# Kernel tuning notes

Measured on AMD Instinct MI355X. Metric: run time of the kernel, lower is better.

Reference implementation:

```python
import jax, jax.numpy as jnp
import numpy as np

SCORE_THRESHOLD = 0.15
IOU_THRESHOLD = 0.5
MAX_OUTPUT = 10          # tf.image.non_max_suppression(..., 10, ...)
NUM_CLASSES = 80
NUM_ANCHORS = 5
NEG = -1e9               # score for suppressed / below-threshold boxes


def setup_inputs() -> dict:
    key = jax.random.key(0)
    k1, k2 = jax.random.split(key)
    preds = jax.random.normal(k1, (16, 52, 52, NUM_ANCHORS * (5 + NUM_CLASSES)), dtype=jnp.float32)
    # anchor priors in grid-cell units, typical YOLOv2 range
    anchors = jax.random.uniform(k2, (NUM_ANCHORS, 2), dtype=jnp.float32, minval=0.5, maxval=6.0)
    return {"preds": preds, "anchors": anchors}


def _decode(preds, anchors):
    """YOLOv2 head decode (the `_interpret_prediction` callable)."""
    B, H, W, _ = preds.shape
    A = anchors.shape[0]
    p = preds.reshape(B, H, W, A, 5 + NUM_CLASSES)
    gy, gx = jnp.meshgrid(jnp.arange(H, dtype=preds.dtype),
                          jnp.arange(W, dtype=preds.dtype), indexing="ij")
    grid = jnp.stack([gx, gy], axis=-1)[None, :, :, None, :]   # (1,H,W,1,2) in (x,y)
    dims = jnp.array([W, H], dtype=preds.dtype)
    box_xy = (jax.nn.sigmoid(p[..., :2]) + grid) / dims        # normalized centers
    box_wh = jnp.exp(p[..., 2:4]) * anchors[None, None, None, :, :] / dims
    box_confidence = jax.nn.sigmoid(p[..., 4:5])
    box_class_probs = jax.nn.softmax(p[..., 5:], axis=-1)
    return box_xy, box_wh, box_confidence, box_class_probs


def _iou(box, boxes):
    """IoU of one box (ymin,xmin,ymax,xmax) against all boxes [N,4]."""
    tl = jnp.maximum(box[:2], boxes[:, :2])
    br = jnp.minimum(box[2:], boxes[:, 2:])
    inter = jnp.prod(jnp.maximum(br - tl, 0.0), axis=-1)
    area1 = jnp.prod(jnp.maximum(box[2:] - box[:2], 0.0))
    area2 = jnp.prod(jnp.maximum(boxes[:, 2:] - boxes[:, :2], 0.0), axis=-1)
    return inter / (area1 + area2 - inter + 1e-9)


def reference(preds, anchors):
    box_xy, box_wh, box_confidence, box_class_probs = _decode(preds, anchors)
    box_mins = box_xy - box_wh / 2.0
    box_maxes = box_xy + box_wh / 2.0
    # (ymin, xmin, ymax, xmax), matching the K.concatenate in the source
    boxes = jnp.concatenate([box_mins[..., 1:2], box_mins[..., 0:1],
                             box_maxes[..., 1:2], box_maxes[..., 0:1]], axis=-1)
    box_scores = box_confidence * box_class_probs
    box_classes = jnp.argmax(box_scores, axis=-1)
    box_class_scores = jnp.max(box_scores, axis=-1)

    boxes = boxes.reshape(-1, 4)                       # [N,4]
    scores = box_class_scores.reshape(-1)              # [N]
    classes = box_classes.reshape(-1).astype(preds.dtype)

    # score-threshold mask: instead of boolean_mask (dynamic shape), kill scores
    live = jnp.where(scores >= SCORE_THRESHOLD, scores, NEG)

    # greedy NMS, fixed MAX_OUTPUT iterations (semantics of tf.image.non_max_suppression)
    def step(cur_scores, _):
        i = jnp.argmax(cur_scores)
        s = cur_scores[i]
        valid = s > NEG / 2
        box = boxes[i]
        ious = _iou(box, boxes)
        nxt = jnp.where(ious > IOU_THRESHOLD, NEG, cur_scores).at[i].set(NEG)
        row = jnp.where(valid,
                        jnp.concatenate([box, s[None], classes[i][None]]),
                        jnp.zeros((6,), dtype=preds.dtype))
        return nxt, row

    _, rows = jax.lax.scan(step, live, None, length=MAX_OUTPUT)
    return rows  # [10, 6] = (ymin, xmin, ymax, xmax, score, class); zero rows = padding
```

## Files before the change

kernel.cpp:

```cpp
#include <hip/hip_runtime.h>
#include <math.h>

#define A_N      5
#define GRID_HW  52
#define NCLS     80
#define CH       85
#define SCORE_T  0.15f
#define IOU_T    0.5f
#define NEGV     (-1e9f)
#define MAXOUT   10

#define WAVES_PB     4
#define BPW          32
#define WAVE_FLOATS  (BPW * CH)
#define WAVE_FULL    10
#define WAVE_TAIL    40

#define NMS_THREADS  256
#define NCAP         4096
#define KR           (NCAP / NMS_THREADS)

__device__ __forceinline__ float fexp(float x) { return __expf(x); }

__device__ __forceinline__ void gload_lds16(const float* g, float* l) {
    __builtin_amdgcn_global_load_lds(
        (const __attribute__((address_space(1))) unsigned int*)g,
        (__attribute__((address_space(3))) unsigned int*)l, 16, 0, 0);
}

__global__ void init_counter_kernel(int* __restrict__ counter) {
    *counter = 0;
}

__global__ __launch_bounds__(256) void decode_kernel(
    const float* __restrict__ preds,
    const float* __restrict__ anchors,
    float4* __restrict__ pbox, float* __restrict__ pscore,
    float* __restrict__ pcls,
    int* __restrict__ counter, int N, int capacity)
{
    __shared__ __align__(16) float lds[WAVES_PB * WAVE_FLOATS];

    const int lane = (int)threadIdx.x & 63;
    const int wid  = (int)threadIdx.x >> 6;
    const int wt   = blockIdx.x * WAVES_PB + wid;
    if (wt * BPW >= N) return;

    const float* gbase = preds + (size_t)wt * WAVE_FLOATS;
    float* lbase = lds + wid * WAVE_FLOATS;

#pragma unroll
    for (int i = 0; i < WAVE_FULL; ++i)
        gload_lds16(gbase + (size_t)(i * 64 + lane) * 4, lbase + i * 256);
    if (lane < WAVE_TAIL)
        gload_lds16(gbase + (size_t)(WAVE_FULL * 64 + lane) * 4,
                    lbase + WAVE_FULL * 256);

    asm volatile("s_waitcnt vmcnt(0)" ::: "memory");
    __builtin_amdgcn_sched_barrier(0);

    const int b  = lane >> 1;
    const int h  = lane & 1;
    const int gi = wt * BPW + b;
    const float* bp = lbase + b * CH;
    const float* cl = bp + 5 + h * 40;

    float s = 0.0f;
    float m = -INFINITY;
    int   am = h * 40;
#pragma unroll
    for (int j = 0; j < 40; ++j) {
        float x = cl[j];
        s += fexp(x);
        if (x > m) { m = x; am = h * 40 + j; }
    }
    {
        float m2 = __shfl_xor(m, 1);
        float s2 = __shfl_xor(s, 1);
        int   am2 = __shfl_xor(am, 1);
        s += s2;
        if (m2 > m || (m2 == m && am2 < am)) { m = m2; am = am2; }
    }

    float conf  = 1.0f / (1.0f + fexp(-bp[4]));
    float score = conf * fexp(m) / s;

    bool live = (h == 0) && (gi < N) && (score >= SCORE_T);

    unsigned long long mask = __ballot(live);
    if (mask) {
        int nlive  = __popcll(mask);
        int leader = (int)__ffsll((long long)mask) - 1;
        int base_ = 0;
        if (lane == leader) base_ = atomicAdd(counter, nlive);
        base_ = __shfl(base_, leader);
        if (live) {
            int a = gi % A_N;
            int t = gi / A_N;
            int wx = t % GRID_HW;
            int hy = (t / GRID_HW) % GRID_HW;
            const float inv = 1.0f / (float)GRID_HW;
            float cx = (1.0f / (1.0f + fexp(-bp[0])) + (float)wx) * inv;
            float cy = (1.0f / (1.0f + fexp(-bp[1])) + (float)hy) * inv;
            float bw = fexp(bp[2]) * anchors[2 * a]     * inv;
            float bh = fexp(bp[3]) * anchors[2 * a + 1] * inv;

            int pos = base_ + __popcll(mask & ((1ull << lane) - 1));
            if (pos < capacity) {
                pbox[pos]   = make_float4(cy - 0.5f * bh, cx - 0.5f * bw,
                                          cy + 0.5f * bh, cx + 0.5f * bw);
                pscore[pos] = score;
                pcls[pos]   = (float)am;
            }
        }
    }
}

__global__ __launch_bounds__(NMS_THREADS) void nms_kernel(
    const float4* __restrict__ pbox, float* __restrict__ pscore,
    const float* __restrict__ pcls, const int* __restrict__ counter,
    int capacity, float* __restrict__ out)
{
    __shared__ float sy0[NCAP], sx0[NCAP], sy1[NCAP], sx1[NCAP], scl[NCAP];
    __shared__ float psc[4];
    __shared__ int   pix[4];
    __shared__ float orow[MAXOUT * 6];

    int M = *counter;
    if (M > capacity) M = capacity;
    const int tid  = (int)threadIdx.x;
    const int lane = tid & 63;
    const int wid  = tid >> 6;

    if (M <= NCAP) {
        float4 rb[KR];
        float  rs[KR];
#pragma unroll
        for (int k = 0; k < KR; ++k) {
            int j = tid + (k << 8);
            if (j < M) {
                float4 b = pbox[j];
                rb[k] = b; rs[k] = pscore[j];
                sy0[j] = b.x; sx0[j] = b.y; sy1[j] = b.z; sx1[j] = b.w;
                scl[j] = pcls[j];
            } else {
                rs[k] = -INFINITY;
                rb[k] = make_float4(0.f, 0.f, 0.f, 0.f);
            }
        }
        __syncthreads();

        for (int it = 0; it < MAXOUT; ++it) {
            float bs = -INFINITY; int bi = -1;
#pragma unroll
            for (int k = 0; k < KR; ++k) {
                if (rs[k] > bs) { bs = rs[k]; bi = tid + (k << 8); }
            }
#pragma unroll
            for (int off = 32; off; off >>= 1) {
                float os = __shfl_xor(bs, off);
                int   oi = __shfl_xor(bi, off);
                if (os > bs || (os == bs && oi != -1 && (bi == -1 || oi < bi))) {
                    bs = os; bi = oi;
                }
            }
            if (lane == 0) { psc[wid] = bs; pix[wid] = bi; }
            __syncthreads();

            bs = psc[0]; bi = pix[0];
#pragma unroll
            for (int w = 1; w < 4; ++w) {
                float os = psc[w]; int oi = pix[w];
                if (os > bs || (os == bs && oi != -1 && (bi == -1 || oi < bi))) {
                    bs = os; bi = oi;
                }
            }
            bool valid = (bi >= 0) && (bs > NEGV * 0.5f);

            if (tid == 0) {
                if (valid) {
                    orow[it*6+0] = sy0[bi]; orow[it*6+1] = sx0[bi];
                    orow[it*6+2] = sy1[bi]; orow[it*6+3] = sx1[bi];
                    orow[it*6+4] = bs;      orow[it*6+5] = scl[bi];
                } else {
                    orow[it*6+0] = 0.f; orow[it*6+1] = 0.f; orow[it*6+2] = 0.f;
                    orow[it*6+3] = 0.f; orow[it*6+4] = 0.f; orow[it*6+5] = 0.f;
                }
            }

            if (valid) {
                float wy0 = sy0[bi], wx0 = sx0[bi];
                float wy1 = sy1[bi], wx1 = sx1[bi];
                float a1 = fmaxf(wy1 - wy0, 0.f) * fmaxf(wx1 - wx0, 0.f);
#pragma unroll
                for (int k = 0; k < KR; ++k) {
                    int j = tid + (k << 8);
                    if (j == bi) rs[k] = NEGV;
                    float ty = fmaxf(wy0, rb[k].x);
                    float tx = fmaxf(wx0, rb[k].y);
                    float by = fminf(wy1, rb[k].z);
                    float bx = fminf(wx1, rb[k].w);
                    float inter = fmaxf(by - ty, 0.f) * fmaxf(bx - tx, 0.f);
                    float a2 = fmaxf(rb[k].z - rb[k].x, 0.f)
                             * fmaxf(rb[k].w - rb[k].y, 0.f);
                    float iou = inter / (a1 + a2 - inter + 1e-9f);
                    if (iou > IOU_T) rs[k] = NEGV;
                }
            }
            __syncthreads();
        }
    } else {
        for (int it = 0; it < MAXOUT; ++it) {
            float bs = -INFINITY; int bi = -1;
            for (int j = tid; j < M; j += NMS_THREADS) {
                float v = pscore[j];
                if (v > bs) { bs = v; bi = j; }
            }
#pragma unroll
            for (int off = 32; off; off >>= 1) {
                float os = __shfl_xor(bs, off);
                int   oi = __shfl_xor(bi, off);
                if (os > bs || (os == bs && oi != -1 && (bi == -1 || oi < bi))) {
                    bs = os; bi = oi;
                }
            }
            if (lane == 0) { psc[wid] = bs; pix[wid] = bi; }
            __syncthreads();
            bs = psc[0]; bi = pix[0];
#pragma unroll
            for (int w = 1; w < 4; ++w) {
                float os = psc[w]; int oi = pix[w];
                if (os > bs || (os == bs && oi != -1 && (bi == -1 || oi < bi))) {
                    bs = os; bi = oi;
                }
            }
            bool valid = (bi >= 0) && (bs > NEGV * 0.5f);
            if (tid == 0) {
                if (valid) {
                    float4 bx = pbox[bi];
                    orow[it*6+0] = bx.x; orow[it*6+1] = bx.y;
                    orow[it*6+2] = bx.z; orow[it*6+3] = bx.w;
                    orow[it*6+4] = bs;   orow[it*6+5] = pcls[bi];
                    pscore[bi] = NEGV;
                } else {
                    orow[it*6+0] = 0.f; orow[it*6+1] = 0.f; orow[it*6+2] = 0.f;
                    orow[it*6+3] = 0.f; orow[it*6+4] = 0.f; orow[it*6+5] = 0.f;
                }
            }
            __syncthreads();
            if (valid) {
                float4 wb = pbox[bi];
                float a1 = fmaxf(wb.z - wb.x, 0.f) * fmaxf(wb.w - wb.y, 0.f);
                for (int j = tid; j < M; j += NMS_THREADS) {
                    float4 bj = pbox[j];
                    float ty = fmaxf(wb.x, bj.x);
                    float tx = fmaxf(wb.y, bj.y);
                    float by = fminf(wb.z, bj.z);
                    float bx = fminf(wb.w, bj.w);
                    float inter = fmaxf(by - ty, 0.f) * fmaxf(bx - tx, 0.f);
                    float a2 = fmaxf(bj.z - bj.x, 0.f) * fmaxf(bj.w - bj.y, 0.f);
                    float iou = inter / (a1 + a2 - inter + 1e-9f);
                    if (iou > IOU_T) pscore[j] = NEGV;
                }
            }
            __syncthreads();
        }
    }

    __syncthreads();
    if (tid < MAXOUT * 6) out[tid] = orow[tid];
}

extern "C" void kernel_launch(void* const* d_in, const int* in_sizes, int n_in,
                              void* d_out, int out_size, void* d_ws, size_t ws_size,
                              hipStream_t stream) {
    (void)n_in; (void)out_size;
    const float* preds   = (const float*)d_in[0];
    const float* anchors = (const float*)d_in[1];
    float* out = (float*)d_out;

    int N = in_sizes[0] / CH;

    char* ws = (char*)d_ws;
    int* counter = (int*)ws;
    size_t avail = (ws_size > 64) ? (ws_size - 64) : 0;
    long long cap = (long long)(avail / (sizeof(float4) + 2 * sizeof(float)));
    if (cap > N) cap = N;
    if (cap < 0) cap = 0;
    int capacity = (int)cap;

    float4* pbox  = (float4*)(ws + 64);
    float* pscore = (float*)(pbox + capacity);
    float* pcls   = pscore + capacity;

    init_counter_kernel<<<1, 1, 0, stream>>>(counter);

    int nBlocks = (N + WAVES_PB * BPW - 1) / (WAVES_PB * BPW);
    decode_kernel<<<nBlocks, 256, 0, stream>>>(
        preds, anchors, pbox, pscore, pcls, counter, N, capacity);
    nms_kernel<<<1, NMS_THREADS, 0, stream>>>(
        pbox, pscore, pcls, counter, capacity, out);
}
```

Measured before the change: 61.59 us.

## Fuse decode and NMS into one kernel via last-block-done atomic

Merges the decode and NMS kernels into a single launch. Each block bumps a done counter, and the last block to finish runs the NMS over the compacted candidates. The NMS path no longer stages box coordinates in shared memory; it keeps them in registers and reads the winning box from global memory. This removes one kernel launch and the gap between kernels, and drops the large shared arrays that would otherwise hurt the decode kernel's occupancy. In exchange, the NMS tail runs serially inside the last block and depends on a threadfence and atomic handshake.

Result: slower. 100.1 us (+62.6%).

```diff
diff --git a/kernel.cpp b/kernel.cpp
--- a/kernel.cpp
+++ b/kernel.cpp
@@ -13,8 +13,8 @@
 #define WAVES_PB     4
 #define BPW          32
 #define WAVE_FLOATS  (BPW * CH)
-#define WAVE_FULL    10
-#define WAVE_TAIL    40
+#define WAVE_F4      (WAVE_FLOATS / 4)
+#define BPB          (WAVES_PB * BPW)
 
 #define NMS_THREADS  256
 #define NCAP         4096
@@ -28,109 +28,119 @@
         (__attribute__((address_space(3))) unsigned int*)l, 16, 0, 0);
 }
 
-__global__ void init_counter_kernel(int* __restrict__ counter) {
-    *counter = 0;
+__global__ void init_counters_kernel(int* __restrict__ counters) {
+    counters[0] = 0;
+    counters[1] = 0;
 }
 
-__global__ __launch_bounds__(256) void decode_kernel(
+__global__ __launch_bounds__(256) void fused_kernel(
     const float* __restrict__ preds,
     const float* __restrict__ anchors,
     float4* __restrict__ pbox, float* __restrict__ pscore,
-    float* __restrict__ pcls,
-    int* __restrict__ counter, int N, int capacity)
+    float* __restrict__ pcls, float* __restrict__ pscratch,
+    int* counters, int N, int capacity, float* __restrict__ out)
 {
-    __shared__ __align__(16) float lds[WAVES_PB * WAVE_FLOATS];
-
-    const int lane = (int)threadIdx.x & 63;
-    const int wid  = (int)threadIdx.x >> 6;
-    const int wt   = blockIdx.x * WAVES_PB + wid;
-    if (wt * BPW >= N) return;
-
-    const float* gbase = preds + (size_t)wt * WAVE_FLOATS;
-    float* lbase = lds + wid * WAVE_FLOATS;
-
-#pragma unroll
-    for (int i = 0; i < WAVE_FULL; ++i)
-        gload_lds16(gbase + (size_t)(i * 64 + lane) * 4, lbase + i * 256);
-    if (lane < WAVE_TAIL)
-        gload_lds16(gbase + (size_t)(WAVE_FULL * 64 + lane) * 4,
-                    lbase + WAVE_FULL * 256);
-
-    asm volatile("s_waitcnt vmcnt(0)" ::: "memory");
-    __builtin_amdgcn_sched_barrier(0);
-
-    const int b  = lane >> 1;
-    const int h  = lane & 1;
-    const int gi = wt * BPW + b;
-    const float* bp = lbase + b * CH;
-    const float* cl = bp + 5 + h * 40;
-
-    float s = 0.0f;
-    float m = -INFINITY;
-    int   am = h * 40;
-#pragma unroll
-    for (int j = 0; j < 40; ++j) {
-        float x = cl[j];
-        s += fexp(x);
-        if (x > m) { m = x; am = h * 40 + j; }
-    }
-    {
-        float m2 = __shfl_xor(m, 1);
-        float s2 = __shfl_xor(s, 1);
-        int   am2 = __shfl_xor(am, 1);
-        s += s2;
-        if (m2 > m || (m2 == m && am2 < am)) { m = m2; am = am2; }
-    }
-
-    float conf  = 1.0f / (1.0f + fexp(-bp[4]));
-    float score = conf * fexp(m) / s;
-
-    bool live = (h == 0) && (gi < N) && (score >= SCORE_T);
-
-    unsigned long long mask = __ballot(live);
-    if (mask) {
-        int nlive  = __popcll(mask);
-        int leader = (int)__ffsll((long long)mask) - 1;
-        int base_ = 0;
-        if (lane == leader) base_ = atomicAdd(counter, nlive);
-        base_ = __shfl(base_, leader);
-        if (live) {
-            int a = gi % A_N;
-            int t = gi / A_N;
-            int wx = t % GRID_HW;
-            int hy = (t / GRID_HW) % GRID_HW;
-            const float inv = 1.0f / (float)GRID_HW;
-            float cx = (1.0f / (1.0f + fexp(-bp[0])) + (float)wx) * inv;
-            float cy = (1.0f / (1.0f + fexp(-bp[1])) + (float)hy) * inv;
-            float bw = fexp(bp[2]) * anchors[2 * a]     * inv;
-            float bh = fexp(bp[3]) * anchors[2 * a + 1] * inv;
-
-            int pos = base_ + __popcll(mask & ((1ull << lane) - 1));
-            if (pos < capacity) {
-                pbox[pos]   = make_float4(cy - 0.5f * bh, cx - 0.5f * bw,
-                                          cy + 0.5f * bh, cx + 0.5f * bw);
-                pscore[pos] = score;
-                pcls[pos]   = (float)am;
-            }
-        }
-    }
-}
-
-__global__ __launch_bounds__(NMS_THREADS) void nms_kernel(
-    const float4* __restrict__ pbox, float* __restrict__ pscore,
-    const float* __restrict__ pcls, const int* __restrict__ counter,
-    int capacity, float* __restrict__ out)
-{
-    __shared__ float sy0[NCAP], sx0[NCAP], sy1[NCAP], sx1[NCAP], scl[NCAP];
+    __shared__ __align__(16) float dlds[WAVES_PB * WAVE_FLOATS];
     __shared__ float psc[4];
     __shared__ int   pix[4];
     __shared__ float orow[MAXOUT * 6];
-
-    int M = *counter;
-    if (M > capacity) M = capacity;
+    __shared__ int   lastFlag;
+
+    int* counter = counters;
+    int* done    = counters + 1;
+
     const int tid  = (int)threadIdx.x;
     const int lane = tid & 63;
     const int wid  = tid >> 6;
+    const int wt   = blockIdx.x * WAVES_PB + wid;
+
+    if ((long long)wt * BPW < N) {
+        const long long total_f4 = ((long long)N * CH) >> 2;
+        const long long base_f4  = (long long)wt * WAVE_F4;
+        float* lbase = dlds + wid * WAVE_FLOATS;
+
+#pragma unroll
+        for (int i = 0; i < 10; ++i) {
+            long long idx = base_f4 + i * 64 + lane;
+            if (idx < total_f4) gload_lds16(preds + idx * 4, lbase + i * 256);
+        }
+        if (lane < 40) {
+            long long idx = base_f4 + 640 + lane;
+            if (idx < total_f4) gload_lds16(preds + idx * 4, lbase + 640 * 4);
+        }
+
+        asm volatile("s_waitcnt vmcnt(0)" ::: "memory");
+        __builtin_amdgcn_sched_barrier(0);
+
+        const int b  = lane >> 1;
+        const int h  = lane & 1;
+        const int gi = wt * BPW + b;
+        const float* bp = lbase + b * CH;
+        const float* cl = bp + 5 + h * 40;
+
+        float s = 0.0f;
+        float m = -INFINITY;
+        int   am = h * 40;
+#pragma unroll
+        for (int j = 0; j < 40; ++j) {
+            float x = cl[j];
+            s += fexp(x);
+            if (x > m) { m = x; am = h * 40 + j; }
+        }
+        {
+            float m2 = __shfl_xor(m, 1);
+            float s2 = __shfl_xor(s, 1);
+            int   am2 = __shfl_xor(am, 1);
+            s += s2;
+            if (m2 > m || (m2 == m && am2 < am)) { m = m2; am = am2; }
+        }
+
+        float conf  = 1.0f / (1.0f + fexp(-bp[4]));
+        float score = conf * fexp(m) / s;
+
+        bool live = (h == 0) && (gi < N) && (score >= SCORE_T);
+
+        unsigned long long mask = __ballot(live);
+        if (mask) {
+            int nlive  = __popcll(mask);
+            int leader = (int)__ffsll((long long)mask) - 1;
+            int base_ = 0;
+            if (lane == leader) base_ = atomicAdd(counter, nlive);
+            base_ = __shfl(base_, leader);
+            if (live) {
+                int a = gi % A_N;
+                int t = gi / A_N;
+                int wx = t % GRID_HW;
+                int hy = (t / GRID_HW) % GRID_HW;
+                const float inv = 1.0f / (float)GRID_HW;
+                float cx = (1.0f / (1.0f + fexp(-bp[0])) + (float)wx) * inv;
+                float cy = (1.0f / (1.0f + fexp(-bp[1])) + (float)hy) * inv;
+                float bw = fexp(bp[2]) * anchors[2 * a]     * inv;
+                float bh = fexp(bp[3]) * anchors[2 * a + 1] * inv;
+
+                int pos = base_ + __popcll(mask & ((1ull << lane) - 1));
+                if (pos < capacity) {
+                    pbox[pos]   = make_float4(cy - 0.5f * bh, cx - 0.5f * bw,
+                                              cy + 0.5f * bh, cx + 0.5f * bw);
+                    pscore[pos] = score;
+                    pcls[pos]   = (float)am;
+                }
+            }
+        }
+    }
+
+    __syncthreads();
+    if (tid == 0) {
+        __threadfence();
+        int prev = atomicAdd(done, 1);
+        lastFlag = (prev == (int)gridDim.x - 1);
+    }
+    __syncthreads();
+    if (!lastFlag) return;
+    __threadfence();
+
+    int M = atomicAdd(counter, 0);
+    if (M > capacity) M = capacity;
 
     if (M <= NCAP) {
         float4 rb[KR];
@@ -138,17 +148,9 @@
 #pragma unroll
         for (int k = 0; k < KR; ++k) {
             int j = tid + (k << 8);
-            if (j < M) {
-                float4 b = pbox[j];
-                rb[k] = b; rs[k] = pscore[j];
-                sy0[j] = b.x; sx0[j] = b.y; sy1[j] = b.z; sx1[j] = b.w;
-                scl[j] = pcls[j];
-            } else {
-                rs[k] = -INFINITY;
-                rb[k] = make_float4(0.f, 0.f, 0.f, 0.f);
-            }
-        }
-        __syncthreads();
+            if (j < M) { rb[k] = pbox[j]; rs[k] = pscore[j]; }
+            else       { rs[k] = -INFINITY; rb[k] = make_float4(0.f,0.f,0.f,0.f); }
+        }
 
         for (int it = 0; it < MAXOUT; ++it) {
             float bs = -INFINITY; int bi = -1;
@@ -177,11 +179,14 @@
             }
             bool valid = (bi >= 0) && (bs > NEGV * 0.5f);
 
+            float4 wb = make_float4(0.f, 0.f, 0.f, 0.f);
+            if (valid) wb = pbox[bi];
+
             if (tid == 0) {
                 if (valid) {
-                    orow[it*6+0] = sy0[bi]; orow[it*6+1] = sx0[bi];
-                    orow[it*6+2] = sy1[bi]; orow[it*6+3] = sx1[bi];
-                    orow[it*6+4] = bs;      orow[it*6+5] = scl[bi];
+                    orow[it*6+0] = wb.x; orow[it*6+1] = wb.y;
+                    orow[it*6+2] = wb.z; orow[it*6+3] = wb.w;
+                    orow[it*6+4] = bs;   orow[it*6+5] = pcls[bi];
                 } else {
                     orow[it*6+0] = 0.f; orow[it*6+1] = 0.f; orow[it*6+2] = 0.f;
                     orow[it*6+3] = 0.f; orow[it*6+4] = 0.f; orow[it*6+5] = 0.f;
@@ -189,17 +194,15 @@
             }
 
             if (valid) {
-                float wy0 = sy0[bi], wx0 = sx0[bi];
-                float wy1 = sy1[bi], wx1 = sx1[bi];
-                float a1 = fmaxf(wy1 - wy0, 0.f) * fmaxf(wx1 - wx0, 0.f);
+                float a1 = fmaxf(wb.z - wb.x, 0.f) * fmaxf(wb.w - wb.y, 0.f);
 #pragma unroll
                 for (int k = 0; k < KR; ++k) {
                     int j = tid + (k << 8);
                     if (j == bi) rs[k] = NEGV;
-                    float ty = fmaxf(wy0, rb[k].x);
-                    float tx = fmaxf(wx0, rb[k].y);
-                    float by = fminf(wy1, rb[k].z);
-                    float bx = fminf(wx1, rb[k].w);
+                    float ty = fmaxf(wb.x, rb[k].x);
+                    float tx = fmaxf(wb.y, rb[k].y);
+                    float by = fminf(wb.z, rb[k].z);
+                    float bx = fminf(wb.w, rb[k].w);
                     float inter = fmaxf(by - ty, 0.f) * fmaxf(bx - tx, 0.f);
                     float a2 = fmaxf(rb[k].z - rb[k].x, 0.f)
                              * fmaxf(rb[k].w - rb[k].y, 0.f);
@@ -210,10 +213,13 @@
             __syncthreads();
         }
     } else {
+        for (int j = tid; j < M; j += NMS_THREADS) pscratch[j] = pscore[j];
+        __syncthreads();
+
         for (int it = 0; it < MAXOUT; ++it) {
             float bs = -INFINITY; int bi = -1;
             for (int j = tid; j < M; j += NMS_THREADS) {
-                float v = pscore[j];
+                float v = pscratch[j];
                 if (v > bs) { bs = v; bi = j; }
             }
 #pragma unroll
@@ -235,13 +241,14 @@
                 }
             }
             bool valid = (bi >= 0) && (bs > NEGV * 0.5f);
+            float4 wb = make_float4(0.f, 0.f, 0.f, 0.f);
+            if (valid) wb = pbox[bi];
             if (tid == 0) {
                 if (valid) {
-                    float4 bx = pbox[bi];
-                    orow[it*6+0] = bx.x; orow[it*6+1] = bx.y;
-                    orow[it*6+2] = bx.z; orow[it*6+3] = bx.w;
+                    orow[it*6+0] = wb.x; orow[it*6+1] = wb.y;
+                    orow[it*6+2] = wb.z; orow[it*6+3] = wb.w;
                     orow[it*6+4] = bs;   orow[it*6+5] = pcls[bi];
-                    pscore[bi] = NEGV;
+                    pscratch[bi] = NEGV;
                 } else {
                     orow[it*6+0] = 0.f; orow[it*6+1] = 0.f; orow[it*6+2] = 0.f;
                     orow[it*6+3] = 0.f; orow[it*6+4] = 0.f; orow[it*6+5] = 0.f;
@@ -249,7 +256,6 @@
             }
             __syncthreads();
             if (valid) {
-                float4 wb = pbox[bi];
                 float a1 = fmaxf(wb.z - wb.x, 0.f) * fmaxf(wb.w - wb.y, 0.f);
                 for (int j = tid; j < M; j += NMS_THREADS) {
                     float4 bj = pbox[j];
@@ -260,7 +266,7 @@
                     float inter = fmaxf(by - ty, 0.f) * fmaxf(bx - tx, 0.f);
                     float a2 = fmaxf(bj.z - bj.x, 0.f) * fmaxf(bj.w - bj.y, 0.f);
                     float iou = inter / (a1 + a2 - inter + 1e-9f);
-                    if (iou > IOU_T) pscore[j] = NEGV;
+                    if (iou > IOU_T) pscratch[j] = NEGV;
                 }
             }
             __syncthreads();
@@ -282,22 +288,22 @@
     int N = in_sizes[0] / CH;
 
     char* ws = (char*)d_ws;
-    int* counter = (int*)ws;
+    int* counters = (int*)ws;
     size_t avail = (ws_size > 64) ? (ws_size - 64) : 0;
-    long long cap = (long long)(avail / (sizeof(float4) + 2 * sizeof(float)));
+    long long cap = (long long)(avail / (sizeof(float4) + 3 * sizeof(float)));
     if (cap > N) cap = N;
     if (cap < 0) cap = 0;
     int capacity = (int)cap;
 
-    float4* pbox  = (float4*)(ws + 64);
-    float* pscore = (float*)(pbox + capacity);
-    float* pcls   = pscore + capacity;
-
-    init_counter_kernel<<<1, 1, 0, stream>>>(counter);
-
-    int nBlocks = (N + WAVES_PB * BPW - 1) / (WAVES_PB * BPW);
-    decode_kernel<<<nBlocks, 256, 0, stream>>>(
-        preds, anchors, pbox, pscore, pcls, counter, N, capacity);
-    nms_kernel<<<1, NMS_THREADS, 0, stream>>>(
-        pbox, pscore, pcls, counter, capacity, out);
+    float4* pbox    = (float4*)(ws + 64);
+    float* pscore   = (float*)(pbox + capacity);
+    float* pcls     = pscore + capacity;
+    float* pscratch = pcls + capacity;
+
+    init_counters_kernel<<<1, 1, 0, stream>>>(counters);
+
+    int nBlocks = (N + BPB - 1) / BPB;
+    fused_kernel<<<nBlocks, 256, 0, stream>>>(
+        preds, anchors, pbox, pscore, pcls, pscratch,
+        counters, N, capacity, out);
 }
```
